# Performance work log

Hardware: AMD Instinct MI355X
Metric: run time of the kernel (lower is better)

The kernel has to match this reference:

```python
import jax, jax.numpy as jnp
import numpy as np
from jax.scipy.special import xlogy

N = 12288
DATA_LEN = 50000
MARGIN = 1.0
GAMMA = 0.1
LAMBDA = 1.0
EPS = 1e-12


def setup_inputs() -> dict:
    key = jax.random.key(0)
    k1, k2, k3 = jax.random.split(key, 3)
    y_pred = jax.random.uniform(k1, (N, 1), dtype=jnp.float32)
    y_pred_adv = jax.random.uniform(k2, (N, 1), dtype=jnp.float32)
    y_true = jax.random.randint(k3, (N,), 0, 2)
    index_s = jnp.arange(N)
    u_all = jnp.zeros((DATA_LEN, 1), dtype=jnp.float32)
    u_pos = jnp.zeros((DATA_LEN, 1), dtype=jnp.float32)
    return {"y_pred": y_pred, "y_pred_adv": y_pred_adv, "u_all": u_all,
            "u_pos": u_pos, "y_true": y_true, "index_s": index_s}


def reference(y_pred, y_pred_adv, u_all, u_pos, y_true, index_s):
    sg = jax.lax.stop_gradient
    f = y_pred[:, 0]                       # [N]
    pos = (y_true == 1)                    # [N] bool
    posf = pos.astype(f.dtype)             # [N]
    # pairwise squared hinge: rows = positives (masked later), cols = all samples
    sur = jnp.square(jnp.maximum(MARGIN - (f[:, None] - f[None, :]), 0.0))  # [N,N]
    row_mean = jnp.mean(sur, axis=1)                       # mean over all samples
    pos_row_mean = jnp.mean(sur * posf[None, :], axis=1)   # mean over positives-as-zeros
    # moving-average buffer update (detached), only at positive rows' indices
    ua = u_all[index_s, 0]
    up = u_pos[index_s, 0]
    ua_new = jnp.where(pos, (1.0 - GAMMA) * ua + GAMMA * sg(row_mean), ua)
    up_new = jnp.where(pos, (1.0 - GAMMA) * up + GAMMA * sg(pos_row_mean), up)
    # p_ij = (u_pos_i - u_all_i * pos_mask_j) / u_all_i^2, detached, rows masked to positives
    denom = jnp.where(pos, jnp.square(ua_new), 1.0)        # guard 0 division on neg rows
    p = (up_new[:, None] - ua_new[:, None] * posf[None, :]) / denom[:, None]
    p = sg(p) * posf[:, None]
    n_pos = jnp.sum(posf)
    nat_loss = jnp.sum(p * sur) / (n_pos * f.shape[0])     # mean over P x N elements
    # adversarial KL (batchmean over first dim)
    y_prob = jnp.concatenate([y_pred, 1.0 - y_pred], axis=-1)          # [N,2]
    y_prob_adv = jnp.concatenate([y_pred_adv, 1.0 - y_pred_adv], axis=-1)
    log_in = jnp.log(y_prob_adv + EPS)
    adv_loss = jnp.sum(xlogy(y_prob, y_prob) - y_prob * log_in) / y_prob.shape[0]
    return nat_loss + LAMBDA * adv_loss
```

## Files before the change

kernel.cpp:

```cpp
#include <hip/hip_runtime.h>
#include <math.h>

#define LAMBDA 1.0
#define EPS 1e-12f

constexpr int BLK      = 1024;
constexpr int MAX_ITER = 12;

__global__ __launch_bounds__(BLK)
void adap_one_block(const float* __restrict__ y_pred,
                    const float* __restrict__ y_pred_adv,
                    const float* __restrict__ u_all,
                    const float* __restrict__ u_pos,
                    const int*  __restrict__ y_true,
                    const int*  __restrict__ index_s,
                    float* __restrict__ out,
                    int n) {
    __shared__ double swred[BLK / 64][8];
    __shared__ double sh[8];

    const int tid  = threadIdx.x;
    const int lane = tid & 63;
    const int wave = tid >> 6;

    double v0 = 0, v1 = 0, v2 = 0, v3 = 0, v4 = 0, v5 = 0;

    auto body1 = [&](int i) {
        const float f   = y_pred[i];
        const int   pos = (y_true[i] == 1);
        const double fd = (double)f;
        v0 += fd; v1 += fd * fd;
        if (pos) { v2 += fd; v3 += fd * fd; v4 += 1.0; }
        const float p  = f;
        const float q  = 1.0f - f;
        const float pa = y_pred_adv[i];
        const float qa = 1.0f - pa;
        float t = 0.0f;
        if (p > 0.0f) t += p * logf(p);
        if (q > 0.0f) t += q * logf(q);
        t -= p * logf(pa + EPS);
        t -= q * logf(qa + EPS);
        v5 += (double)t;
    };

    #pragma unroll
    for (int k = 0; k < MAX_ITER; ++k) {
        const int i = k * BLK + tid;
        if (i < n) body1(i);
    }
    for (int i = MAX_ITER * BLK + tid; i < n; i += BLK) body1(i);

    for (int off = 32; off > 0; off >>= 1) {
        v0 += __shfl_down(v0, off, 64);
        v1 += __shfl_down(v1, off, 64);
        v2 += __shfl_down(v2, off, 64);
        v3 += __shfl_down(v3, off, 64);
        v4 += __shfl_down(v4, off, 64);
        v5 += __shfl_down(v5, off, 64);
    }
    if (lane == 0) {
        swred[wave][0] = v0; swred[wave][1] = v1; swred[wave][2] = v2;
        swred[wave][3] = v3; swred[wave][4] = v4; swred[wave][5] = v5;
    }
    __syncthreads();
    if (tid < 6) {
        double a = 0.0;
        #pragma unroll
        for (int w = 0; w < BLK / 64; ++w) a += swred[w][tid];
        sh[tid] = a;
    }
    __syncthreads();
    const double S1 = sh[0], S2 = sh[1], S1p = sh[2], S2p = sh[3];
    const double Np = sh[4], adv = sh[5];

    double csum = 0.0;
    const double nd = (double)n;

    auto body2 = [&](int i) {
        if (y_true[i] == 1) {
            const double f = (double)y_pred[i];
            const int  idx = index_s[i];
            const double ua = (double)u_all[idx];
            const double up = (double)u_pos[idx];
            const double a  = 1.0 - f;
            const double row_sum     = nd * a * a + 2.0 * a * S1  + S2;
            const double pos_row_sum = Np * a * a + 2.0 * a * S1p + S2p;
            const double ua_new = 0.9 * ua + 0.1 * (row_sum / nd);
            const double up_new = 0.9 * up + 0.1 * (pos_row_sum / nd);
            csum += (up_new * row_sum - ua_new * pos_row_sum) / (ua_new * ua_new);
        }
    };

    #pragma unroll
    for (int k = 0; k < MAX_ITER; ++k) {
        const int i = k * BLK + tid;
        if (i < n) body2(i);
    }
    for (int i = MAX_ITER * BLK + tid; i < n; i += BLK) body2(i);

    for (int off = 32; off > 0; off >>= 1) csum += __shfl_down(csum, off, 64);
    if (lane == 0) swred[wave][0] = csum;
    __syncthreads();

    if (tid == 0) {
        double a = 0.0;
        #pragma unroll
        for (int w = 0; w < BLK / 64; ++w) a += swred[w][0];
        const double nat_loss = a / (Np * nd);
        const double adv_loss = adv / nd;
        out[0] = (float)(nat_loss + LAMBDA * adv_loss);
    }
}

extern "C" void kernel_launch(void* const* d_in, const int* in_sizes, int n_in,
                              void* d_out, int out_size, void* d_ws, size_t ws_size,
                              hipStream_t stream) {
    const float* y_pred     = (const float*)d_in[0];
    const float* y_pred_adv = (const float*)d_in[1];
    const float* u_all      = (const float*)d_in[2];
    const float* u_pos      = (const float*)d_in[3];
    const int*   y_true     = (const int*)d_in[4];
    const int*   index_s    = (const int*)d_in[5];
    float* out = (float*)d_out;
    const int n = in_sizes[0];

    (void)d_ws; (void)ws_size;

    adap_one_block<<<1, BLK, 0, stream>>>(y_pred, y_pred_adv, u_all, u_pos,
                                          y_true, index_s, out, n);
}
```

Before: 81.85 us.

## Split loss kernel across multiple blocks with last-block atomic reduction

Replaces the single-block kernel with a multi-block grid. Each block redundantly computes the global first and second moment sums using float4 loads, so that the KL term and the per-positive moving-average term can be split across blocks. A final block, picked through an atomic counter in the workspace, adds up the per-block partials. This spreads the logf-heavy work over many compute units, at the cost of repeated moment scans and a counter protocol that assumes the workspace starts out holding a specific poison value.

```diff
diff --git a/kernel.cpp b/kernel.cpp
--- a/kernel.cpp
+++ b/kernel.cpp
@@ -4,35 +4,67 @@
 #define LAMBDA 1.0
 #define EPS 1e-12f
 
-constexpr int BLK      = 1024;
-constexpr int MAX_ITER = 12;
+
+constexpr int BLK  = 512;
+constexpr int MAXB = 64;
+constexpr unsigned POISON = 0xAAAAAAAAu;
 
 __global__ __launch_bounds__(BLK)
-void adap_one_block(const float* __restrict__ y_pred,
-                    const float* __restrict__ y_pred_adv,
-                    const float* __restrict__ u_all,
-                    const float* __restrict__ u_pos,
-                    const int*  __restrict__ y_true,
-                    const int*  __restrict__ index_s,
-                    float* __restrict__ out,
-                    int n) {
+void adap_fused(const float* __restrict__ y_pred,
+                const float* __restrict__ y_pred_adv,
+                const float* __restrict__ u_all,
+                const float* __restrict__ u_pos,
+                const int*  __restrict__ y_true,
+                const int*  __restrict__ index_s,
+                double* __restrict__ part,
+                unsigned* __restrict__ counter,
+                float* __restrict__ out,
+                int n) {
     __shared__ double swred[BLK / 64][8];
     __shared__ double sh[8];
 
+    const int nb   = gridDim.x;
+    const int b    = blockIdx.x;
     const int tid  = threadIdx.x;
     const int lane = tid & 63;
     const int wave = tid >> 6;
 
-    double v0 = 0, v1 = 0, v2 = 0, v3 = 0, v4 = 0, v5 = 0;
+    double s1 = 0, s2 = 0, s1p = 0, s2p = 0, np = 0;
+    const int n4 = n & ~3;
+    for (int base = tid * 4; base < n4; base += BLK * 4) {
+        const float4 fv = *reinterpret_cast<const float4*>(y_pred + base);
+        const int4   tv = *reinterpret_cast<const int4*>(y_true + base);
+        {
+            const double fd = (double)fv.x;
+            s1 += fd; s2 += fd * fd;
+            if (tv.x == 1) { s1p += fd; s2p += fd * fd; np += 1.0; }
+        }
+        {
+            const double fd = (double)fv.y;
+            s1 += fd; s2 += fd * fd;
+            if (tv.y == 1) { s1p += fd; s2p += fd * fd; np += 1.0; }
+        }
+        {
+            const double fd = (double)fv.z;
+            s1 += fd; s2 += fd * fd;
+            if (tv.z == 1) { s1p += fd; s2p += fd * fd; np += 1.0; }
+        }
+        {
+            const double fd = (double)fv.w;
+            s1 += fd; s2 += fd * fd;
+            if (tv.w == 1) { s1p += fd; s2p += fd * fd; np += 1.0; }
+        }
+    }
+    for (int i = n4 + tid; i < n; i += BLK) {
+        const double fd = (double)y_pred[i];
+        s1 += fd; s2 += fd * fd;
+        if (y_true[i] == 1) { s1p += fd; s2p += fd * fd; np += 1.0; }
+    }
 
-    auto body1 = [&](int i) {
-        const float f   = y_pred[i];
-        const int   pos = (y_true[i] == 1);
-        const double fd = (double)f;
-        v0 += fd; v1 += fd * fd;
-        if (pos) { v2 += fd; v3 += fd * fd; v4 += 1.0; }
-        const float p  = f;
-        const float q  = 1.0f - f;
+    double advp = 0.0;
+    for (int i = b * BLK + tid; i < n; i += nb * BLK) {
+        const float p  = y_pred[i];
+        const float q  = 1.0f - p;
         const float pa = y_pred_adv[i];
         const float qa = 1.0f - pa;
         float t = 0.0f;
@@ -40,16 +72,10 @@
         if (q > 0.0f) t += q * logf(q);
         t -= p * logf(pa + EPS);
         t -= q * logf(qa + EPS);
-        v5 += (double)t;
-    };
+        advp += (double)t;
+    }
 
-    #pragma unroll
-    for (int k = 0; k < MAX_ITER; ++k) {
-        const int i = k * BLK + tid;
-        if (i < n) body1(i);
-    }
-    for (int i = MAX_ITER * BLK + tid; i < n; i += BLK) body1(i);
-
+    double v0 = s1, v1 = s2, v2 = s1p, v3 = s2p, v4 = np, v5 = advp;
     for (int off = 32; off > 0; off >>= 1) {
         v0 += __shfl_down(v0, off, 64);
         v1 += __shfl_down(v1, off, 64);
@@ -71,44 +97,52 @@
     }
     __syncthreads();
     const double S1 = sh[0], S2 = sh[1], S1p = sh[2], S2p = sh[3];
-    const double Np = sh[4], adv = sh[5];
+    const double Np = sh[4];
 
     double csum = 0.0;
     const double nd = (double)n;
-
-    auto body2 = [&](int i) {
+    for (int i = b * BLK + tid; i < n; i += nb * BLK) {
         if (y_true[i] == 1) {
-            const double f = (double)y_pred[i];
-            const int  idx = index_s[i];
-            const double ua = (double)u_all[idx];
-            const double up = (double)u_pos[idx];
-            const double a  = 1.0 - f;
+            const double f   = (double)y_pred[i];
+            const int    idx = index_s[i];
+            const double ua  = (double)u_all[idx];
+            const double up  = (double)u_pos[idx];
+            const double a   = 1.0 - f;
             const double row_sum     = nd * a * a + 2.0 * a * S1  + S2;
             const double pos_row_sum = Np * a * a + 2.0 * a * S1p + S2p;
             const double ua_new = 0.9 * ua + 0.1 * (row_sum / nd);
             const double up_new = 0.9 * up + 0.1 * (pos_row_sum / nd);
             csum += (up_new * row_sum - ua_new * pos_row_sum) / (ua_new * ua_new);
         }
-    };
-
-    #pragma unroll
-    for (int k = 0; k < MAX_ITER; ++k) {
-        const int i = k * BLK + tid;
-        if (i < n) body2(i);
     }
-    for (int i = MAX_ITER * BLK + tid; i < n; i += BLK) body2(i);
-
     for (int off = 32; off > 0; off >>= 1) csum += __shfl_down(csum, off, 64);
     if (lane == 0) swred[wave][0] = csum;
     __syncthreads();
 
     if (tid == 0) {
-        double a = 0.0;
+        double c = 0.0;
         #pragma unroll
-        for (int w = 0; w < BLK / 64; ++w) a += swred[w][0];
-        const double nat_loss = a / (Np * nd);
-        const double adv_loss = adv / nd;
-        out[0] = (float)(nat_loss + LAMBDA * adv_loss);
+        for (int w = 0; w < BLK / 64; ++w) c += swred[w][0];
+        __hip_atomic_store(&part[b * 2 + 0], c,
+                           __ATOMIC_RELAXED, __HIP_MEMORY_SCOPE_AGENT);
+        __hip_atomic_store(&part[b * 2 + 1], sh[5],
+                           __ATOMIC_RELAXED, __HIP_MEMORY_SCOPE_AGENT);
+        const unsigned old = __hip_atomic_fetch_add(
+            counter, 1u, __ATOMIC_ACQ_REL, __HIP_MEMORY_SCOPE_AGENT);
+        if (old == POISON + (unsigned)nb - 1u) {
+            double ctot = 0.0, atot = 0.0;
+            for (int k = 0; k < nb; ++k) {
+                ctot += __hip_atomic_load(&part[k * 2 + 0],
+                                          __ATOMIC_RELAXED, __HIP_MEMORY_SCOPE_AGENT);
+                atot += __hip_atomic_load(&part[k * 2 + 1],
+                                          __ATOMIC_RELAXED, __HIP_MEMORY_SCOPE_AGENT);
+            }
+            const double nat_loss = ctot / (Np * nd);
+            const double adv_loss = atot / nd;
+            out[0] = (float)(nat_loss + LAMBDA * adv_loss);
+            __hip_atomic_store(counter, POISON,
+                               __ATOMIC_RELAXED, __HIP_MEMORY_SCOPE_AGENT);
+        }
     }
 }
 
@@ -124,8 +158,12 @@
     float* out = (float*)d_out;
     const int n = in_sizes[0];
 
-    (void)d_ws; (void)ws_size;
+    double*   part    = (double*)d_ws;
+    unsigned* counter = (unsigned*)((char*)d_ws + MAXB * 2 * sizeof(double));
 
-    adap_one_block<<<1, BLK, 0, stream>>>(y_pred, y_pred_adv, u_all, u_pos,
-                                          y_true, index_s, out, n);
+    int nb = (n + BLK - 1) / BLK;
+    if (nb > MAXB) nb = MAXB;
+
+    adap_fused<<<nb, BLK, 0, stream>>>(y_pred, y_pred_adv, u_all, u_pos,
+                                       y_true, index_s, part, counter, out, n);
 }
```

Result: faster. 72.10 us (-11.9%).
